# Kernel optimization log

Measured on AMD Instinct MI355X. Metric: run time of the kernel, lower is better.

The kernel has to match this reference:

```python
import jax, jax.numpy as jnp
import numpy as np
from jax import lax

TEMPERATURE = 0.5
MOMENTUM = 0.9
EPS = 1e-12  # F.normalize eps

B, D, K = 8192, 512, 16384


def _l2norm(x):
    # matches F.normalize(p=2): x / max(||x||, eps)
    n = jnp.sqrt(jnp.sum(x * x, axis=-1, keepdims=True))
    return x / jnp.maximum(n, EPS)


def setup_inputs() -> dict:
    key = jax.random.key(0)
    k1, k2, k3 = jax.random.split(key, 3)
    embeddings = jax.random.normal(k1, (B, D), dtype=jnp.float32)
    cluster_ids = jax.random.randint(k2, (B,), 0, K, dtype=jnp.int64)
    prototypes = jax.random.normal(k3, (K, D), dtype=jnp.float32)
    return {"embeddings": embeddings, "cluster_ids": cluster_ids, "prototypes": prototypes}


def reference(embeddings, cluster_ids, prototypes):
    emb_n = _l2norm(embeddings)            # [B, D]
    proto_n = _l2norm(prototypes)          # [K, D]
    sim = jnp.einsum('bd,kd->bk', emb_n, proto_n) / TEMPERATURE  # [B, K]

    pos = jnp.take_along_axis(sim, cluster_ids[:, None], axis=1)  # [B, 1]
    # mask out the positive column, then stable logsumexp over negatives
    is_pos = jnp.arange(sim.shape[1])[None, :] == cluster_ids[:, None]  # [B, K]
    neg = jnp.where(is_pos, -jnp.inf, sim)
    lse = jax.scipy.special.logsumexp(neg, axis=1, keepdims=True)       # [B, 1]
    loss = jnp.mean(-pos + lse)

    # serial momentum EMA update (order-dependent for duplicate cluster ids)
    def step(protos, xc):
        x, c = xc
        row = MOMENTUM * protos[c] + (1.0 - MOMENTUM) * x
        return protos.at[c].set(row), None

    new_protos, _ = lax.scan(step, prototypes, (embeddings, cluster_ids))
    return loss, new_protos
```

## Files before the change

kernel.cpp:

```cpp
#include <hip/hip_runtime.h>
#include <hip/hip_bf16.h>


#define B_N 8192
#define D_N 512
#define K_N 16384
#define INV_T 2.0f
#define MOM 0.9f

#define BM 128
#define BKF 128
#define BTR 256
#define KSPLIT 4
#define NTILE 16
#define CAP 64

typedef __attribute__((ext_vector_type(8))) int intx8;
typedef __attribute__((ext_vector_type(4))) float floatx4;

__device__ __forceinline__ void gl_lds16(const void* g, void* lds) {
    __builtin_amdgcn_global_load_lds(
        (const __attribute__((address_space(1))) void*)g,
        (__attribute__((address_space(3))) void*)lds, 16, 0, 0);
}

__device__ __forceinline__ intx8 frag2(const unsigned char* rp, int o0, int o1) {
    intx8 v;
    ((int4*)&v)[0] = *(const int4*)(rp + o0);
    ((int4*)&v)[1] = *(const int4*)(rp + o1);
    return v;
}

__global__ void norm_kernel(const float* __restrict__ emb, const float* __restrict__ pro,
                            unsigned char* __restrict__ embq, unsigned char* __restrict__ proq,
                            float* __restrict__ rowsum, float* __restrict__ out) {
    if (blockIdx.x < 32) rowsum[blockIdx.x * 256 + threadIdx.x] = 0.0f;
    if (blockIdx.x == 32 && threadIdx.x == 0) out[0] = 0.0f;
    int row = blockIdx.x * 4 + (threadIdx.x >> 6);
    int lane = threadIdx.x & 63;
    const float* x;
    unsigned char* o;
    if (row < B_N) {
        x = emb + (size_t)row * D_N;
        o = embq + (size_t)row * D_N;
    } else {
        x = pro + (size_t)(row - B_N) * D_N;
        o = proq + (size_t)(row - B_N) * D_N;
    }
    const float4* xp = (const float4*)(x + lane * 8);
    float4 v0 = xp[0];
    float4 v1 = xp[1];
    float ss = v0.x * v0.x + v0.y * v0.y + v0.z * v0.z + v0.w * v0.w +
               v1.x * v1.x + v1.y * v1.y + v1.z * v1.z + v1.w * v1.w;
    #pragma unroll
    for (int of = 32; of; of >>= 1) ss += __shfl_xor(ss, of);
    float sc = 16.0f / fmaxf(sqrtf(ss), 1e-12f);
    int w0 = 0, w1 = 0;
    w0 = __builtin_amdgcn_cvt_pk_fp8_f32(v0.x * sc, v0.y * sc, w0, false);
    w0 = __builtin_amdgcn_cvt_pk_fp8_f32(v0.z * sc, v0.w * sc, w0, true);
    w1 = __builtin_amdgcn_cvt_pk_fp8_f32(v1.x * sc, v1.y * sc, w1, false);
    w1 = __builtin_amdgcn_cvt_pk_fp8_f32(v1.z * sc, v1.w * sc, w1, true);
    int2 st = {w0, w1};
    *(int2*)(o + lane * 8) = st;
}

__global__ void pos_kernel(const float* __restrict__ emb, const float* __restrict__ pro,
                           const int* __restrict__ cid, float* __restrict__ rowpos) {
    int b = blockIdx.x * 4 + (threadIdx.x >> 6);
    int lane = threadIdx.x & 63;
    int c = cid[b];
    const float4* ep = (const float4*)(emb + (size_t)b * D_N + lane * 8);
    const float4* pp = (const float4*)(pro + (size_t)c * D_N + lane * 8);
    float4 e0 = ep[0], e1 = ep[1], p0 = pp[0], p1 = pp[1];
    float dp = e0.x * p0.x + e0.y * p0.y + e0.z * p0.z + e0.w * p0.w +
               e1.x * p1.x + e1.y * p1.y + e1.z * p1.z + e1.w * p1.w;
    float ee = e0.x * e0.x + e0.y * e0.y + e0.z * e0.z + e0.w * e0.w +
               e1.x * e1.x + e1.y * e1.y + e1.z * e1.z + e1.w * e1.w;
    float qq = p0.x * p0.x + p0.y * p0.y + p0.z * p0.z + p0.w * p0.w +
               p1.x * p1.x + p1.y * p1.y + p1.z * p1.z + p1.w * p1.w;
    #pragma unroll
    for (int o = 32; o; o >>= 1) {
        dp += __shfl_xor(dp, o);
        ee += __shfl_xor(ee, o);
        qq += __shfl_xor(qq, o);
    }
    if (lane == 0)
        rowpos[b] = INV_T * dp / (fmaxf(sqrtf(ee), 1e-12f) * fmaxf(sqrtf(qq), 1e-12f));
}

#define FLASH_STEP(CH, AFC, AFN)                                                      \
    do {                                                                              \
        const unsigned char* rb = Bs[(CH) & 1] + (size_t)(wn * 64 + lcol) * BKF;      \
        intx8 bf[4];                                                                  \
        _Pragma("unroll")                                                             \
        for (int j = 0; j < 4; j++)                                                   \
            bf[j] = frag2(rb + j * (16 * BKF), fsw0, fsw1);                           \
        if (tt < NTILE - 1 || (CH) < 3) {                                             \
            const unsigned char* ran = aF + ((((CH) + 1) & 3) << 7);                  \
            _Pragma("unroll")                                                         \
            for (int i = 0; i < 4; i++)                                               \
                AFN[i] = frag2(ran + i * (16 * D_N), fsw0, fsw1);                     \
        }                                                                             \
        __builtin_amdgcn_s_setprio(1);                                                \
        _Pragma("unroll")                                                             \
        for (int i = 0; i < 4; i++)                                                   \
            _Pragma("unroll")                                                         \
            for (int j = 0; j < 4; j++)                                               \
                acc[i][j] = __builtin_amdgcn_mfma_scale_f32_16x16x128_f8f6f4(         \
                    AFC[i], bf[j], acc[i][j], 0, 0, 0, 0x7F7F7F7F, 0, 0x7F7F7F7F);    \
        __builtin_amdgcn_s_setprio(0);                                                \
        if ((CH) == 3) {                                                              \
            _Pragma("unroll")                                                         \
            for (int i = 0; i < 4; i++)                                               \
                _Pragma("unroll")                                                     \
                for (int j = 0; j < 4; j++)                                           \
                    _Pragma("unroll")                                                 \
                    for (int r = 0; r < 4; r++) {                                     \
                        rs[i * 4 + r] += __expf(acc[i][j][r] * (INV_T / 256.0f));     \
                        acc[i][j][r] = 0.0f;                                          \
                    }                                                                 \
        }                                                                             \
        __builtin_amdgcn_s_barrier();                                                 \
        if (tt < NTILE - 1 || (CH) < 2) {                                             \
            const unsigned char* s =                                                  \
                bT + (((CH) >= 2) ? (size_t)BTR * D_N : 0) + ((((CH) + 2) & 3) << 7); \
            unsigned char* d = (unsigned char*)Bs[(CH) & 1] + ldsW;                   \
            _Pragma("unroll")                                                         \
            for (int p = 0; p < 4; p++)                                               \
                gl_lds16(s + (size_t)p * 64 * D_N, d + p * 8192);                     \
            asm volatile("s_waitcnt vmcnt(4)" ::: "memory");                          \
        } else {                                                                      \
            asm volatile("s_waitcnt vmcnt(0)" ::: "memory");                          \
        }                                                                             \
        __builtin_amdgcn_s_barrier();                                                 \
    } while (0)

__global__ __launch_bounds__(512, 2) void flash_kernel(const unsigned char* __restrict__ embq,
                                                       const unsigned char* __restrict__ proq,
                                                       float* __restrict__ rowsum_g) {
    __shared__ __align__(16) unsigned char As[BM * D_N];
    __shared__ __align__(16) unsigned char Bs[2][BTR * BKF];
    const int t = threadIdx.x;
    const int w = t >> 6, lane = t & 63;
    const int quad = lane >> 4, lcol = lane & 15;
    const int wm = w >> 2, wn = w & 3;
    const int rowBase = blockIdx.x * BM;
    const int kb = blockIdx.y * (K_N / KSPLIT);

    const int fsw0 = (((quad << 1) | 0) ^ (lcol & 7)) << 4;
    const int fsw1 = (((quad << 1) | 1) ^ (lcol & 7)) << 4;
    const unsigned char* aF = As + (size_t)(wm * 64 + lcol) * D_N;
    const int ldsW = w * 1024;

    const int aRow = w * 2 + (lane >> 5);
    const unsigned char* aS = embq + (size_t)(rowBase + aRow) * D_N +
                              (((lane >> 3) & 3) << 7) + (((lane & 7) ^ (aRow & 7)) << 4);
    const unsigned char* bS = proq + (size_t)(kb + w * 8 + (lane >> 3)) * D_N +
                              (((lane & 7) ^ ((lane >> 3) & 7)) << 4);

    floatx4 acc[4][4];
    float rs[16];
    #pragma unroll
    for (int i = 0; i < 4; i++)
        #pragma unroll
        for (int j = 0; j < 4; j++) {
            floatx4 z = {0.0f, 0.0f, 0.0f, 0.0f};
            acc[i][j] = z;
        }
    #pragma unroll
    for (int i = 0; i < 16; i++) rs[i] = 0.0f;

    #pragma unroll
    for (int p = 0; p < 8; p++)
        gl_lds16(aS + p * 8192, As + p * 8192 + ldsW);
    #pragma unroll
    for (int p = 0; p < 4; p++)
        gl_lds16(bS + (size_t)p * 64 * D_N, Bs[0] + p * 8192 + ldsW);
    #pragma unroll
    for (int p = 0; p < 4; p++)
        gl_lds16(bS + (size_t)p * 64 * D_N + BKF, Bs[1] + p * 8192 + ldsW);
    asm volatile("s_waitcnt vmcnt(4)" ::: "memory");
    __builtin_amdgcn_s_barrier();

    intx8 af0[4], af1[4];
    #pragma unroll
    for (int i = 0; i < 4; i++)
        af0[i] = frag2(aF + i * (16 * D_N), fsw0, fsw1);

    const unsigned char* bT = bS;
    for (int tt = 0; tt < NTILE; tt++) {
        FLASH_STEP(0, af0, af1);
        FLASH_STEP(1, af1, af0);
        FLASH_STEP(2, af0, af1);
        FLASH_STEP(3, af1, af0);
        bT += (size_t)BTR * D_N;
    }

    #pragma unroll
    for (int i = 0; i < 16; i++) {
        #pragma unroll
        for (int o = 1; o < 16; o <<= 1) rs[i] += __shfl_xor(rs[i], o);
    }
    if (lcol == 0) {
        #pragma unroll
        for (int i = 0; i < 4; i++)
            #pragma unroll
            for (int r = 0; r < 4; r++)
                atomicAdd(&rowsum_g[rowBase + wm * 64 + i * 16 + quad * 4 + r],
                          rs[i * 4 + r]);
    }
}

__global__ void loss_kernel(const float* __restrict__ rowsum, const float* __restrict__ rowpos,
                            float* __restrict__ out, int* __restrict__ cnt) {
    __shared__ float red[256];
    int t = threadIdx.x;
    int b = blockIdx.x * 256 + t;
    cnt[b * 2] = 0;
    cnt[b * 2 + 1] = 0;
    float p = rowpos[b];
    red[t] = logf(rowsum[b] - __expf(p)) - p;
    __syncthreads();
    for (int o = 128; o; o >>= 1) {
        if (t < o) red[t] += red[t + o];
        __syncthreads();
    }
    if (t == 0) atomicAdd(out, red[0] * (1.0f / (float)B_N));
}

__global__ void ema_count(const int* __restrict__ cid, int* __restrict__ cnt,
                          int* __restrict__ bucket) {
    int b = blockIdx.x * 256 + threadIdx.x;
    int c = cid[b];
    int slot = atomicAdd(&cnt[c], 1);
    if (slot < CAP) bucket[c * CAP + slot] = b;
}

__global__ void ema_apply(const float* __restrict__ emb, const float* __restrict__ pro,
                          const int* __restrict__ cnt, const int* __restrict__ bucket,
                          float* __restrict__ outp) {
    int k = blockIdx.x * 4 + (threadIdx.x >> 6);
    int lane = threadIdx.x & 63;
    int n = cnt[k];
    n = n < CAP ? n : CAP;
    const float4* pp = (const float4*)(pro + (size_t)k * D_N + lane * 8);
    float4 a0 = pp[0], a1 = pp[1];
    int myb = (lane < n) ? bucket[k * CAP + lane] : 0x7fffffff;
    for (int i = 0; i < n; i++) {
        int m = myb;
        #pragma unroll
        for (int o = 1; o < 64; o <<= 1) {
            int v = __shfl_xor(m, o);
            m = v < m ? v : m;
        }
        const float4* ep = (const float4*)(emb + (size_t)m * D_N + lane * 8);
        float4 e0 = ep[0], e1 = ep[1];
        a0.x = MOM * a0.x + (1.0f - MOM) * e0.x;
        a0.y = MOM * a0.y + (1.0f - MOM) * e0.y;
        a0.z = MOM * a0.z + (1.0f - MOM) * e0.z;
        a0.w = MOM * a0.w + (1.0f - MOM) * e0.w;
        a1.x = MOM * a1.x + (1.0f - MOM) * e1.x;
        a1.y = MOM * a1.y + (1.0f - MOM) * e1.y;
        a1.z = MOM * a1.z + (1.0f - MOM) * e1.z;
        a1.w = MOM * a1.w + (1.0f - MOM) * e1.w;
        if (myb == m) myb = 0x7fffffff;
    }
    float4* op = (float4*)(outp + (size_t)k * D_N + lane * 8);
    op[0] = a0;
    op[1] = a1;
}

extern "C" void kernel_launch(void* const* d_in, const int* in_sizes, int n_in,
                              void* d_out, int out_size, void* d_ws, size_t ws_size,
                              hipStream_t stream) {
    const float* emb = (const float*)d_in[0];
    const int* cid = (const int*)d_in[1];
    const float* pro = (const float*)d_in[2];
    float* out = (float*)d_out;

    char* ws = (char*)d_ws;
    unsigned char* embq = (unsigned char*)ws;
    unsigned char* proq = (unsigned char*)(ws + 4194304);
    float* rowsum = (float*)(ws + 12582912);
    float* rowpos = (float*)(ws + 12615680);
    int* cnt = (int*)(ws + 4194304);
    int* bucket = (int*)(ws + 4194304 + 65536);

    norm_kernel<<<(B_N + K_N) / 4, 256, 0, stream>>>(emb, pro, embq, proq, rowsum, out);
    pos_kernel<<<B_N / 4, 256, 0, stream>>>(emb, pro, cid, rowpos);
    flash_kernel<<<dim3(B_N / BM, KSPLIT), 512, 0, stream>>>(embq, proq, rowsum);
    loss_kernel<<<B_N / 256, 256, 0, stream>>>(rowsum, rowpos, out, cnt);
    ema_count<<<B_N / 256, 256, 0, stream>>>(cid, cnt, bucket);
    ema_apply<<<K_N / 4, 256, 0, stream>>>(emb, pro, cnt, bucket, out + 1);
}
```

Measured before the change: 200.3 us.

## Keep A fragments in registers and triple-buffer B tiles with one barrier

The whole A (embedding) tile for each wave is now loaded straight from global memory into registers once, so the 64KB A region in LDS goes away. The B (prototype) staging moves from two LDS buffers to a three-buffer ring. The next load is issued at the start of each step, and only one barrier per step remains instead of two. B fragment reads are split into two halves interleaved with MFMA groups, which cuts register pressure and removes LDS traffic for A, but keeps 64 extra VGPRs of A fragments live, which may hurt occupancy at 2 blocks/CU.

```diff
diff --git a/kernel.cpp b/kernel.cpp
--- a/kernel.cpp
+++ b/kernel.cpp
@@ -13,6 +13,8 @@
 #define BTR 256
 #define KSPLIT 4
 #define NTILE 16
+#define NCH 64
+#define BUFB 32768
 #define CAP 64
 
 typedef __attribute__((ext_vector_type(8))) int intx8;
@@ -88,28 +90,48 @@
         rowpos[b] = INV_T * dp / (fmaxf(sqrtf(ee), 1e-12f) * fmaxf(sqrtf(qq), 1e-12f));
 }
 
-#define FLASH_STEP(CH, AFC, AFN)                                                      \
+#define FSTEP(CH)                                                                     \
     do {                                                                              \
-        const unsigned char* rb = Bs[(CH) & 1] + (size_t)(wn * 64 + lcol) * BKF;      \
-        intx8 bf[4];                                                                  \
-        _Pragma("unroll")                                                             \
-        for (int j = 0; j < 4; j++)                                                   \
-            bf[j] = frag2(rb + j * (16 * BKF), fsw0, fsw1);                           \
-        if (tt < NTILE - 1 || (CH) < 3) {                                             \
-            const unsigned char* ran = aF + ((((CH) + 1) & 3) << 7);                  \
+        const int cc = tt * 4 + (CH);                                                 \
+        const int bW = bR >= BUFB ? bR - BUFB : bR + 2 * BUFB;                        \
+        if (tt < NTILE - 1 || (CH) < 2) {                                             \
+                              \
+            const unsigned char* s = bS + (size_t)(((cc + 2) >> 2) * BTR) * D_N +     \
+                                     ((((CH) + 2) & 3) << 7);                         \
+            unsigned char* d = Bs + bW + ldsW;                                        \
             _Pragma("unroll")                                                         \
-            for (int i = 0; i < 4; i++)                                               \
-                AFN[i] = frag2(ran + i * (16 * D_N), fsw0, fsw1);                     \
+            for (int p = 0; p < 4; p++)                                               \
+                gl_lds16(s + (size_t)p * 64 * D_N, d + p * 8192);                     \
         }                                                                             \
+        const unsigned char* rb = Bs + bR + (wn * 64 + lcol) * BKF;                   \
+        intx8 bf2[2];                                                                 \
+        bf2[0] = frag2(rb + 0 * (16 * BKF), fsw0, fsw1);                              \
+        bf2[1] = frag2(rb + 1 * (16 * BKF), fsw0, fsw1);                              \
+        asm volatile("s_waitcnt lgkmcnt(0)" ::: "memory");                            \
+        __builtin_amdgcn_sched_barrier(0);                                            \
         __builtin_amdgcn_s_setprio(1);                                                \
         _Pragma("unroll")                                                             \
         for (int i = 0; i < 4; i++)                                                   \
             _Pragma("unroll")                                                         \
-            for (int j = 0; j < 4; j++)                                               \
+            for (int j = 0; j < 2; j++)                                               \
                 acc[i][j] = __builtin_amdgcn_mfma_scale_f32_16x16x128_f8f6f4(         \
-                    AFC[i], bf[j], acc[i][j], 0, 0, 0, 0x7F7F7F7F, 0, 0x7F7F7F7F);    \
+                    afr[(CH)][i], bf2[j], acc[i][j], 0, 0, 0, 0x7F7F7F7F, 0,          \
+                    0x7F7F7F7F);                                                      \
         __builtin_amdgcn_s_setprio(0);                                                \
-        if ((CH) == 3) {                                                              \
+        bf2[0] = frag2(rb + 2 * (16 * BKF), fsw0, fsw1);                              \
+        bf2[1] = frag2(rb + 3 * (16 * BKF), fsw0, fsw1);                              \
+        asm volatile("s_waitcnt lgkmcnt(0)" ::: "memory");                            \
+        __builtin_amdgcn_sched_barrier(0);                                            \
+        __builtin_amdgcn_s_setprio(1);                                                \
+        _Pragma("unroll")                                                             \
+        for (int i = 0; i < 4; i++)                                                   \
+            _Pragma("unroll")                                                         \
+            for (int j = 0; j < 2; j++)                                               \
+                acc[i][2 + j] = __builtin_amdgcn_mfma_scale_f32_16x16x128_f8f6f4(     \
+                    afr[(CH)][i], bf2[j], acc[i][2 + j], 0, 0, 0, 0x7F7F7F7F, 0,      \
+                    0x7F7F7F7F);                                                      \
+        __builtin_amdgcn_s_setprio(0);                                                \
+        if ((CH) == 3) {     \
             _Pragma("unroll")                                                         \
             for (int i = 0; i < 4; i++)                                               \
                 _Pragma("unroll")                                                     \
@@ -120,26 +142,18 @@
                         acc[i][j][r] = 0.0f;                                          \
                     }                                                                 \
         }                                                                             \
+        if (tt < NTILE - 1 || (CH) < 2)                                               \
+            asm volatile("s_waitcnt vmcnt(4)" ::: "memory");                          \
+        else                                                                          \
+            asm volatile("s_waitcnt vmcnt(0)" ::: "memory");                          \
         __builtin_amdgcn_s_barrier();                                                 \
-        if (tt < NTILE - 1 || (CH) < 2) {                                             \
-            const unsigned char* s =                                                  \
-                bT + (((CH) >= 2) ? (size_t)BTR * D_N : 0) + ((((CH) + 2) & 3) << 7); \
-            unsigned char* d = (unsigned char*)Bs[(CH) & 1] + ldsW;                   \
-            _Pragma("unroll")                                                         \
-            for (int p = 0; p < 4; p++)                                               \
-                gl_lds16(s + (size_t)p * 64 * D_N, d + p * 8192);                     \
-            asm volatile("s_waitcnt vmcnt(4)" ::: "memory");                          \
-        } else {                                                                      \
-            asm volatile("s_waitcnt vmcnt(0)" ::: "memory");                          \
-        }                                                                             \
-        __builtin_amdgcn_s_barrier();                                                 \
+        bR = bR == 2 * BUFB ? 0 : bR + BUFB;                                          \
     } while (0)
 
 __global__ __launch_bounds__(512, 2) void flash_kernel(const unsigned char* __restrict__ embq,
                                                        const unsigned char* __restrict__ proq,
                                                        float* __restrict__ rowsum_g) {
-    __shared__ __align__(16) unsigned char As[BM * D_N];
-    __shared__ __align__(16) unsigned char Bs[2][BTR * BKF];
+    __shared__ __align__(16) unsigned char Bs[3 * BUFB];
     const int t = threadIdx.x;
     const int w = t >> 6, lane = t & 63;
     const int quad = lane >> 4, lcol = lane & 15;
@@ -149,12 +163,8 @@
 
     const int fsw0 = (((quad << 1) | 0) ^ (lcol & 7)) << 4;
     const int fsw1 = (((quad << 1) | 1) ^ (lcol & 7)) << 4;
-    const unsigned char* aF = As + (size_t)(wm * 64 + lcol) * D_N;
     const int ldsW = w * 1024;
 
-    const int aRow = w * 2 + (lane >> 5);
-    const unsigned char* aS = embq + (size_t)(rowBase + aRow) * D_N +
-                              (((lane >> 3) & 3) << 7) + (((lane & 7) ^ (aRow & 7)) << 4);
     const unsigned char* bS = proq + (size_t)(kb + w * 8 + (lane >> 3)) * D_N +
                               (((lane & 7) ^ ((lane >> 3) & 7)) << 4);
 
@@ -170,30 +180,34 @@
     #pragma unroll
     for (int i = 0; i < 16; i++) rs[i] = 0.0f;
 
-    #pragma unroll
-    for (int p = 0; p < 8; p++)
-        gl_lds16(aS + p * 8192, As + p * 8192 + ldsW);
+    intx8 afr[4][4];
+    {
+        const unsigned char* aBase =
+            embq + (size_t)(rowBase + wm * 64 + lcol) * D_N + quad * 32;
+        #pragma unroll
+        for (int ch = 0; ch < 4; ch++)
+            #pragma unroll
+            for (int i = 0; i < 4; i++) {
+                const unsigned char* p = aBase + (size_t)i * (16 * D_N) + (ch << 7);
+                ((int4*)&afr[ch][i])[0] = *(const int4*)(p);
+                ((int4*)&afr[ch][i])[1] = *(const int4*)(p + 16);
+            }
+    }
     #pragma unroll
     for (int p = 0; p < 4; p++)
-        gl_lds16(bS + (size_t)p * 64 * D_N, Bs[0] + p * 8192 + ldsW);
+        gl_lds16(bS + (size_t)p * 64 * D_N, Bs + p * 8192 + ldsW);
     #pragma unroll
     for (int p = 0; p < 4; p++)
-        gl_lds16(bS + (size_t)p * 64 * D_N + BKF, Bs[1] + p * 8192 + ldsW);
+        gl_lds16(bS + (size_t)p * 64 * D_N + BKF, Bs + BUFB + p * 8192 + ldsW);
     asm volatile("s_waitcnt vmcnt(4)" ::: "memory");
     __builtin_amdgcn_s_barrier();
 
-    intx8 af0[4], af1[4];
-    #pragma unroll
-    for (int i = 0; i < 4; i++)
-        af0[i] = frag2(aF + i * (16 * D_N), fsw0, fsw1);
-
-    const unsigned char* bT = bS;
+    int bR = 0;
     for (int tt = 0; tt < NTILE; tt++) {
-        FLASH_STEP(0, af0, af1);
-        FLASH_STEP(1, af1, af0);
-        FLASH_STEP(2, af0, af1);
-        FLASH_STEP(3, af1, af0);
-        bT += (size_t)BTR * D_N;
+        FSTEP(0);
+        FSTEP(1);
+        FSTEP(2);
+        FSTEP(3);
     }
 
     #pragma unroll
```

After: 211.1 us. +5.4%, slower.
